# Performance work log

Measured on AMD Instinct MI355X. Metric: run time of the kernel, lower is better.

## Reference

```python
import jax, jax.numpy as jnp
import numpy as np

N = 5000
NFEAT = 512
NHID = 64
NHEADS = 8
NCLASS = 40
ALPHA = 0.2  # leaky relu slope
NEG_INF = -9e15


def setup_inputs() -> dict:
    key = jax.random.key(0)
    ks = jax.random.split(key, 12)
    x = jax.random.normal(ks[0], (N, NFEAT), dtype=jnp.float32)
    # binary adjacency, ~32 avg degree, with self loops
    adj = (jax.random.uniform(ks[1], (N, N)) < (32.0 / N)).astype(jnp.float32)
    adj = jnp.maximum(adj, jnp.eye(N, dtype=jnp.float32))
    s = 1.0 / np.sqrt(NFEAT)
    W_h = jax.random.uniform(ks[2], (NHEADS, NFEAT, NHID), minval=-s, maxval=s, dtype=jnp.float32)
    a_h = jax.random.uniform(ks[3], (NHEADS, 2 * NHID), minval=-s, maxval=s, dtype=jnp.float32)
    s2 = 1.0 / np.sqrt(NHID * NHEADS)
    W_o = jax.random.uniform(ks[4], (NHID * NHEADS, NHID), minval=-s2, maxval=s2, dtype=jnp.float32)
    a_o = jax.random.uniform(ks[5], (2 * NHID,), minval=-s2, maxval=s2, dtype=jnp.float32)
    s3 = 1.0 / np.sqrt(NHID)
    fc1_w = jax.random.uniform(ks[6], (NHID, 200), minval=-s3, maxval=s3, dtype=jnp.float32)
    fc1_b = jax.random.uniform(ks[7], (200,), minval=-s3, maxval=s3, dtype=jnp.float32)
    s4 = 1.0 / np.sqrt(200)
    fc2_w = jax.random.uniform(ks[8], (200, NCLASS), minval=-s4, maxval=s4, dtype=jnp.float32)
    fc2_b = jax.random.uniform(ks[9], (NCLASS,), minval=-s4, maxval=s4, dtype=jnp.float32)
    return {"x": x, "adj": adj, "W_h": W_h, "a_h": a_h, "W_o": W_o, "a_o": a_o,
            "fc1_w": fc1_w, "fc1_b": fc1_b, "fc2_w": fc2_w, "fc2_b": fc2_b}


def _masked_attention(e, adj):
    # e: [..., N, N]; mask where adj == 0, then row softmax
    e = jnp.where(adj > 0, e, NEG_INF)
    return jax.nn.softmax(e, axis=-1)


def reference(x, adj, W_h, a_h, W_o, a_o, fc1_w, fc1_b, fc2_w, fc2_b):
    # ---- multi-head GAT layer (concat=True), eval mode (dropout off) ----
    Wh = jnp.einsum('nf,hfo->hno', x, W_h)                 # [H, N, nhid]
    f1 = jnp.einsum('hno,ho->hn', Wh, a_h[:, :NHID])       # [H, N]
    f2 = jnp.einsum('hno,ho->hn', Wh, a_h[:, NHID:])       # [H, N]
    e = jax.nn.leaky_relu(f1[:, :, None] + f2[:, None, :], ALPHA)  # [H, N, N]
    att = _masked_attention(e, adj[None, :, :])
    h = jnp.einsum('hnm,hmo->hno', att, Wh)                # [H, N, nhid]
    h1 = jax.nn.elu(h).transpose(1, 0, 2).reshape(N, NHEADS * NHID)  # concat heads

    # ---- output GAT layer (concat=False) ----
    Wh2 = h1 @ W_o                                         # [N, nhid]
    g1 = Wh2 @ a_o[:NHID]                                  # [N]
    g2 = Wh2 @ a_o[NHID:]                                  # [N]
    e2 = jax.nn.leaky_relu(g1[:, None] + g2[None, :], ALPHA)
    att2 = _masked_attention(e2, adj)
    h2 = att2 @ Wh2                                        # [N, nhid]

    # ---- MLP head ----
    h3 = jax.nn.elu(h2 @ fc1_w + fc1_b)
    return h3 @ fc2_w + fc2_b                              # [N, nclass]
```

## Files before the change

kernel.cpp:

```cpp
#include <hip/hip_runtime.h>

typedef unsigned short u16;
typedef unsigned int u32;
typedef unsigned long long u64;
typedef __bf16 bf16_t;
typedef __bf16 bf16x8 __attribute__((ext_vector_type(8)));
typedef float f32x4 __attribute__((ext_vector_type(4)));
typedef u32 u32x4 __attribute__((ext_vector_type(4)));

#define NN 5000
#define NF 512
#define NH 64
#define HEADS 8
#define NCLS 40
#define CAP 128
#define LRELU 0.2f
#define BMW 80

#define CVT_BIG 320
#define BM_BLKS 1250
#define CVT_GRID (CVT_BIG + 8 + BM_BLKS)

__device__ __forceinline__ bool adj_is_bf16(const void* adj) {
    return ((*(const u32*)adj) & 0xFFFFu) != 0u;
}
__device__ __forceinline__ u16 rne_bf16(float f) {
    u32 u = __float_as_uint(f);
    u += 0x7FFFu + ((u >> 16) & 1u);
    return (u16)(u >> 16);
}
__device__ __forceinline__ float up_bf16(u16 h) {
    return __uint_as_float((u32)h << 16);
}
__device__ __forceinline__ u32x4 ntload4(const void* p, int idx) {
    return __builtin_nontemporal_load(((const u32x4*)p) + idx);
}

__global__ __launch_bounds__(256) void cvt(const void* __restrict__ x, const void* __restrict__ W_h,
                                           const void* __restrict__ adj,
                                           const void* a_h, const void* W_o, const void* a_o,
                                           const void* f1w, const void* f1b,
                                           const void* f2w, const void* f2b,
                                           u16* __restrict__ xc, u16* __restrict__ whc,
                                           float* a_hc, float* W_oc, float* a_oc,
                                           float* f1wc, float* f1bc, float* f2wc, float* f2bc,
                                           u64* __restrict__ bm) {
    const bool isb = adj_is_bf16(adj);
    const int b = blockIdx.x;
    if (b < CVT_BIG) {
        const int X4 = NN * NF / 4;
        const int T4 = X4 + HEADS * NF * NH / 4;
        for (int i = b * 256 + threadIdx.x; i < T4; i += CVT_BIG * 256) {
            const void* src; u16* dst; int off;
            if (i < X4) { src = x; dst = xc; off = i; }
            else        { src = W_h; dst = whc; off = i - X4; }
            ushort4 o;
            if (isb) {
                o = ((const ushort4*)src)[off];
            } else {
                u32x4 vv = ntload4(src, off);
                o.x = rne_bf16(__uint_as_float(vv[0])); o.y = rne_bf16(__uint_as_float(vv[1]));
                o.z = rne_bf16(__uint_as_float(vv[2])); o.w = rne_bf16(__uint_as_float(vv[3]));
            }
            ((ushort4*)dst)[off] = o;
        }
    } else if (b < CVT_BIG + 8) {
        const int s0 = HEADS * 2 * NH, s1 = HEADS * NH * NH, s2 = 2 * NH,
                  s3 = NH * 200, s4 = 200, s5 = 200 * NCLS, s6 = NCLS;
        const int total = s0 + s1 + s2 + s3 + s4 + s5 + s6;
        for (int i = (b - CVT_BIG) * 256 + threadIdx.x; i < total; i += 8 * 256) {
            const void* src; float* dst; int off = i;
            if (off < s0) { src = a_h; dst = a_hc; }
            else if ((off -= s0) < s1) { src = W_o;  dst = W_oc; }
            else if ((off -= s1) < s2) { src = a_o;  dst = a_oc; }
            else if ((off -= s2) < s3) { src = f1w;  dst = f1wc; }
            else if ((off -= s3) < s4) { src = f1b;  dst = f1bc; }
            else if ((off -= s4) < s5) { src = f2w;  dst = f2wc; }
            else { off -= s5;           src = f2b;  dst = f2bc; }
            dst[off] = isb ? up_bf16(((const u16*)src)[off]) : ((const float*)src)[off];
        }
    } else {
        const int lane = threadIdx.x & 63;
        const int wid  = threadIdx.x >> 6;
        const int r = (b - CVT_BIG - 8) * 4 + wid;
        u64* bmrow = bm + (size_t)r * BMW;
        if (!isb) {
            const float* row = (const float*)adj + (size_t)r * NN;
            #pragma unroll
            for (int pass = 0; pass < 2; ++pass) {
                u32x4 v[10];
                #pragma unroll
                for (int k = 0; k < 10; ++k) {
                    int c = (pass * 10 + k) * 64 + lane;
                    v[k] = (c < 1250) ? ntload4(row, c) : (u32x4){0u, 0u, 0u, 0u};
                }
                #pragma unroll
                for (int k = 0; k < 10; ++k) {
                    int i = pass * 10 + k;
                    #pragma unroll
                    for (int j = 0; j < 4; ++j) {
                        u64 m = __ballot(v[k][j] != 0u);
                        if (lane == j) bmrow[i * 4 + j] = m;
                    }
                }
            }
        } else {
            const u16* row = (const u16*)adj + (size_t)r * NN;
            u32x4 v[10];
            #pragma unroll
            for (int k = 0; k < 10; ++k) {
                int c = k * 64 + lane;
                v[k] = (c < 625) ? ntload4(row, c) : (u32x4){0u, 0u, 0u, 0u};
            }
            #pragma unroll
            for (int k = 0; k < 10; ++k) {
                #pragma unroll
                for (int j = 0; j < 4; ++j) {
                    u64 mlo = __ballot((v[k][j] & 0xFFFFu) != 0u);
                    u64 mhi = __ballot((v[k][j] >> 16) != 0u);
                    if (lane == 2 * j)     bmrow[k * 8 + 2 * j]     = mlo;
                    if (lane == 2 * j + 1) bmrow[k * 8 + 2 * j + 1] = mhi;
                }
            }
        }
    }
}

__global__ __launch_bounds__(256) void gemm1_f(const bf16_t* __restrict__ x,
                                               const bf16_t* __restrict__ W_h,
                                               const float* __restrict__ a_h,
                                               float* __restrict__ Wh,
                                               float* __restrict__ f1,
                                               float* __restrict__ f2) {
    const int lane = threadIdx.x & 63;
    const int wid  = threadIdx.x >> 6;
    const int rg = blockIdx.x;
    const int h  = blockIdx.y;
    const int quad = lane >> 4;
    const int lr   = lane & 15;
    const int kq   = quad * 8;
    const int nCol = wid * 16 + lr;
    const bf16_t* Bh = W_h + (size_t)h * NF * NH;
    __shared__ float f1s[4][64], f2s[4][64];

    bf16x8 bfrag[16];
    #pragma unroll
    for (int s = 0; s < 16; ++s) {
        bf16x8 bb;
        #pragma unroll
        for (int j = 0; j < 8; ++j) bb[j] = Bh[(s * 32 + kq + j) * NH + nCol];
        bfrag[s] = bb;
    }
    const float a1c = a_h[h * 128 + nCol];
    const float a2c = a_h[h * 128 + NH + nCol];

    for (int t = 0; t < 4; ++t) {
        const int rb = rg * 64 + t * 16;
        int row  = rb + lr;
        int rowc = row < NN ? row : NN - 1;
        const bf16_t* xp = x + (size_t)rowc * NF + kq;
        f32x4 acc = {0.f, 0.f, 0.f, 0.f};
        #pragma unroll
        for (int s = 0; s < 16; ++s) {
            bf16x8 a = *(const bf16x8*)(xp + s * 32);
            acc = __builtin_amdgcn_mfma_f32_16x16x32_bf16(a, bfrag[s], acc, 0, 0, 0);
        }
        #pragma unroll
        for (int r = 0; r < 4; ++r) {
            int gr = rb + quad * 4 + r;
            if (gr < NN) Wh[(size_t)gr * (HEADS * NH) + h * NH + nCol] = acc[r];
            float p1 = acc[r] * a1c, p2 = acc[r] * a2c;
            #pragma unroll
            for (int o = 8; o; o >>= 1) { p1 += __shfl_xor(p1, o); p2 += __shfl_xor(p2, o); }
            if (lr == 0) { f1s[wid][t * 16 + quad * 4 + r] = p1; f2s[wid][t * 16 + quad * 4 + r] = p2; }
        }
    }
    __syncthreads();
    if (wid == 0) {
        int gr = rg * 64 + lane;
        if (gr < NN) {
            f1[h * NN + gr] = f1s[0][lane] + f1s[1][lane] + f1s[2][lane] + f1s[3][lane];
            f2[h * NN + gr] = f2s[0][lane] + f2s[1][lane] + f2s[2][lane] + f2s[3][lane];
        }
    }
}

__global__ __launch_bounds__(256) void agg1f(const void* __restrict__ adj,
                                             const u64* __restrict__ bm,
                                             const float* __restrict__ Wh,
                                             const float* __restrict__ f1,
                                             const float* __restrict__ f2,
                                             int* __restrict__ nbr, int* __restrict__ deg,
                                             float* __restrict__ h1) {
    const bool isb = adj_is_bf16(adj);
    const int lane = threadIdx.x & 63;
    const int wid  = threadIdx.x >> 6;
    const int n = blockIdx.x;
    __shared__ int s_nbr[CAP];
    __shared__ int s_dall;

    if (wid == 0) {
        const u64* bmrow = bm + (size_t)n * BMW;
        int base = 0;
        #pragma unroll
        for (int r2 = 0; r2 < 2; ++r2) {
            int w = r2 * 64 + lane;
            u64 mw = (w < BMW) ? bmrow[w] : 0ull;
            int pc = __popcll(mw);
            int scan = pc;
            #pragma unroll
            for (int o = 1; o < 64; o <<= 1) {
                int t = __shfl_up(scan, o);
                if (lane >= o) scan += t;
            }
            int off = base + scan - pc;
            while (mw) {
                int bb = __ffsll(mw) - 1;
                mw &= mw - 1;
                int elem;
                if (!isb) elem = ((w >> 2) * 64 + bb) * 4 + (w & 3);
                else      elem = ((w >> 3) * 64 + bb) * 8 + (w & 7);
                if (off < CAP) s_nbr[off] = elem;
                ++off;
            }
            base += __shfl(scan, 63);
        }
        if (lane == 0) s_dall = base < CAP ? base : CAP;
    }
    __syncthreads();
    const int dall = s_dall;
    for (int i = threadIdx.x; i < dall; i += 256) nbr[(size_t)n * CAP + i] = s_nbr[i];
    if (threadIdx.x == 0) deg[n] = dall;

    const int ha = wid, hb = wid + 4;
    const int nb0 = (lane < dall) ? s_nbr[lane] : 0;
    const int nb1 = (lane + 64 < dall) ? s_nbr[lane + 64] : 0;
    const float f10 = f1[ha * NN + n], f11 = f1[hb * NN + n];
    const float* f2ha = f2 + (size_t)ha * NN;
    const float* f2hb = f2 + (size_t)hb * NN;

    float e00 = -INFINITY, e01 = -INFINITY, e10 = -INFINITY, e11 = -INFINITY;
    if (lane < dall) {
        float a = f10 + f2ha[nb0]; e00 = a > 0.f ? a : LRELU * a;
        float b = f11 + f2hb[nb0]; e10 = b > 0.f ? b : LRELU * b;
    }
    if (lane + 64 < dall) {
        float a = f10 + f2ha[nb1]; e01 = a > 0.f ? a : LRELU * a;
        float b = f11 + f2hb[nb1]; e11 = b > 0.f ? b : LRELU * b;
    }
    float mx0 = fmaxf(e00, e01), mx1 = fmaxf(e10, e11);
    #pragma unroll
    for (int o = 32; o; o >>= 1) {
        mx0 = fmaxf(mx0, __shfl_xor(mx0, o));
        mx1 = fmaxf(mx1, __shfl_xor(mx1, o));
    }
    float p00 = lane < dall ? expf(e00 - mx0) : 0.f;
    float p01 = lane + 64 < dall ? expf(e01 - mx0) : 0.f;
    float p10 = lane < dall ? expf(e10 - mx1) : 0.f;
    float p11 = lane + 64 < dall ? expf(e11 - mx1) : 0.f;
    float sm0 = p00 + p01, sm1 = p10 + p11;
    #pragma unroll
    for (int o = 32; o; o >>= 1) { sm0 += __shfl_xor(sm0, o); sm1 += __shfl_xor(sm1, o); }

    float A0 = 0.f, A1 = 0.f, A2 = 0.f, A3 = 0.f;
    float B0 = 0.f, B1 = 0.f, B2 = 0.f, B3 = 0.f;
    const float* W0 = Wh + ha * NH + lane;
    const float* W1 = Wh + hb * NH + lane;
    int j = 0;
    for (; j + 4 <= dall; j += 4) {
        #pragma unroll
        for (int i = 0; i < 4; ++i) {
            int jj = j + i;
            int sl = jj & 63;
            bool lo = jj < 64;
            int   m  = lo ? __shfl(nb0, sl) : __shfl(nb1, sl);
            float a0 = lo ? __shfl(p00, sl) : __shfl(p01, sl);
            float a1 = lo ? __shfl(p10, sl) : __shfl(p11, sl);
            size_t base = (size_t)m * (HEADS * NH);
            float w0 = W0[base], w1 = W1[base];
            if (i == 0) { A0 += a0 * w0; B0 += a1 * w1; }
            else if (i == 1) { A1 += a0 * w0; B1 += a1 * w1; }
            else if (i == 2) { A2 += a0 * w0; B2 += a1 * w1; }
            else { A3 += a0 * w0; B3 += a1 * w1; }
        }
    }
    for (; j < dall; ++j) {
        int sl = j & 63;
        bool lo = j < 64;
        int   m  = lo ? __shfl(nb0, sl) : __shfl(nb1, sl);
        float a0 = lo ? __shfl(p00, sl) : __shfl(p01, sl);
        float a1 = lo ? __shfl(p10, sl) : __shfl(p11, sl);
        size_t base = (size_t)m * (HEADS * NH);
        A0 += a0 * W0[base]; B0 += a1 * W1[base];
    }
    float hv0 = (A0 + A1 + A2 + A3) / sm0;
    float hv1 = (B0 + B1 + B2 + B3) / sm1;
    hv0 = hv0 > 0.f ? hv0 : expf(hv0) - 1.f;
    hv1 = hv1 > 0.f ? hv1 : expf(hv1) - 1.f;
    h1[(size_t)n * (HEADS * NH) + ha * NH + lane] = hv0;
    h1[(size_t)n * (HEADS * NH) + hb * NH + lane] = hv1;
}

__global__ __launch_bounds__(256) void gemm2_4(const float* __restrict__ h1,
                                               const float* __restrict__ W_o,
                                               const float* __restrict__ a_o,
                                               float* __restrict__ Wh2,
                                               float* __restrict__ g1,
                                               float* __restrict__ g2) {
    const int t = threadIdx.x;
    const int n0 = blockIdx.x * 4;
    __shared__ float sh[4 * 512];
    __shared__ float ps[4][4][64];
    const float4* src = (const float4*)(h1 + (size_t)n0 * 512);
    ((float4*)sh)[t]       = src[t];
    ((float4*)sh)[t + 256] = src[t + 256];
    __syncthreads();
    const int o = t & 63, part = t >> 6;
    float a0 = 0.f, a1 = 0.f, a2 = 0.f, a3 = 0.f;
    const float* wo = W_o + part * 128 * 64 + o;
    const float* s0 = sh + part * 128;
    #pragma unroll 4
    for (int f = 0; f < 128; ++f) {
        float w = wo[f * 64];
        a0 += s0[f] * w; a1 += s0[512 + f] * w; a2 += s0[1024 + f] * w; a3 += s0[1536 + f] * w;
    }
    ps[part][0][o] = a0; ps[part][1][o] = a1; ps[part][2][o] = a2; ps[part][3][o] = a3;
    __syncthreads();
    const int nd = t >> 6;
    float w2 = ps[0][nd][o] + ps[1][nd][o] + ps[2][nd][o] + ps[3][nd][o];
    Wh2[(size_t)(n0 + nd) * 64 + o] = w2;
    float p1 = w2 * a_o[o], p2 = w2 * a_o[64 + o];
    #pragma unroll
    for (int s = 32; s; s >>= 1) { p1 += __shfl_xor(p1, s); p2 += __shfl_xor(p2, s); }
    if (o == 0) { g1[n0 + nd] = p1; g2[n0 + nd] = p2; }
}

__global__ __launch_bounds__(256) void agg2_mlp(const float* __restrict__ Wh2,
                                                const float* __restrict__ g1,
                                                const float* __restrict__ g2,
                                                const int* __restrict__ nbr,
                                                const int* __restrict__ deg,
                                                const float* __restrict__ fc1_w,
                                                const float* __restrict__ fc1_b,
                                                const float* __restrict__ fc2_w,
                                                const float* __restrict__ fc2_b,
                                                float* __restrict__ out) {
    const int lane = threadIdx.x & 63;
    const int wid  = threadIdx.x >> 6;
    const int t = threadIdx.x;
    const int n0 = blockIdx.x * 4;
    const int n = n0 + wid;
    __shared__ float s_alpha[4][CAP];
    __shared__ int   s_nbr[4][CAP];
    __shared__ float s_h2[4][NH];
    __shared__ float s_h3[4][200];
    __shared__ float ps2[2][4][NCLS];
    const int d = deg[n];
    const int* nb = nbr + (size_t)n * CAP;
    const float gn = g1[n];

    float mx = -INFINITY;
    for (int j = lane; j < d; j += 64) {
        int m = nb[j];
        s_nbr[wid][j] = m;
        float e = gn + g2[m];
        e = e > 0.f ? e : LRELU * e;
        s_alpha[wid][j] = e;
        mx = fmaxf(mx, e);
    }
    #pragma unroll
    for (int o = 32; o; o >>= 1) mx = fmaxf(mx, __shfl_xor(mx, o));
    float sm = 0.f;
    for (int j = lane; j < d; j += 64) {
        float p = expf(s_alpha[wid][j] - mx);
        s_alpha[wid][j] = p;
        sm += p;
    }
    #pragma unroll
    for (int o = 32; o; o >>= 1) sm += __shfl_xor(sm, o);

    float acc0 = 0.f, acc1 = 0.f, acc2 = 0.f, acc3 = 0.f;
    int j = 0;
    for (; j + 4 <= d; j += 4) {
        acc0 += s_alpha[wid][j]     * Wh2[(size_t)s_nbr[wid][j]     * NH + lane];
        acc1 += s_alpha[wid][j + 1] * Wh2[(size_t)s_nbr[wid][j + 1] * NH + lane];
        acc2 += s_alpha[wid][j + 2] * Wh2[(size_t)s_nbr[wid][j + 2] * NH + lane];
        acc3 += s_alpha[wid][j + 3] * Wh2[(size_t)s_nbr[wid][j + 3] * NH + lane];
    }
    for (; j < d; ++j) acc0 += s_alpha[wid][j] * Wh2[(size_t)s_nbr[wid][j] * NH + lane];
    s_h2[wid][lane] = (acc0 + acc1 + acc2 + acc3) / sm;
    __syncthreads();

    if (t < 200) {
        float b0 = 0.f, b1 = 0.f, b2 = 0.f, b3 = 0.f;
        #pragma unroll 4
        for (int f = 0; f < NH; ++f) {
            float w = fc1_w[f * 200 + t];
            b0 += s_h2[0][f] * w; b1 += s_h2[1][f] * w; b2 += s_h2[2][f] * w; b3 += s_h2[3][f] * w;
        }
        float bb = fc1_b[t];
        b0 += bb; b1 += bb; b2 += bb; b3 += bb;
        s_h3[0][t] = b0 > 0.f ? b0 : expf(b0) - 1.f;
        s_h3[1][t] = b1 > 0.f ? b1 : expf(b1) - 1.f;
        s_h3[2][t] = b2 > 0.f ? b2 : expf(b2) - 1.f;
        s_h3[3][t] = b3 > 0.f ? b3 : expf(b3) - 1.f;
    }
    __syncthreads();

    if (t < 80) {
        const int o = t % 40, fh = t / 40;
        float c0 = 0.f, c1 = 0.f, c2 = 0.f, c3 = 0.f;
        #pragma unroll 4
        for (int f = fh * 100; f < fh * 100 + 100; ++f) {
            float w = fc2_w[f * NCLS + o];
            c0 += s_h3[0][f] * w; c1 += s_h3[1][f] * w; c2 += s_h3[2][f] * w; c3 += s_h3[3][f] * w;
        }
        ps2[fh][0][o] = c0; ps2[fh][1][o] = c1; ps2[fh][2][o] = c2; ps2[fh][3][o] = c3;
    }
    __syncthreads();
    if (t < 160) {
        const int nd = t / 40, o = t % 40;
        out[(size_t)(n0 + nd) * NCLS + o] = ps2[0][nd][o] + ps2[1][nd][o] + fc2_b[o];
    }
}

extern "C" void kernel_launch(void* const* d_in, const int* in_sizes, int n_in,
                              void* d_out, int out_size, void* d_ws, size_t ws_size,
                              hipStream_t stream) {
    const void* x     = d_in[0];
    const void* adj   = d_in[1];
    const void* W_h   = d_in[2];
    const void* a_h   = d_in[3];
    const void* W_o   = d_in[4];
    const void* a_o   = d_in[5];
    const void* fc1_w = d_in[6];
    const void* fc1_b = d_in[7];
    const void* fc2_w = d_in[8];
    const void* fc2_b = d_in[9];
    float* out = (float*)d_out;

    char* ws = (char*)d_ws;
    int*   nbr   = (int*)(ws + 0);
    int*   deg   = (int*)(ws + 2560000);
    float* Wh    = (float*)(ws + 2580000);
    float* f1    = (float*)(ws + 12820000);
    float* f2    = (float*)(ws + 12980000);
    float* h1    = (float*)(ws + 13140000);
    float* Wh2   = (float*)(ws + 23380000);
    float* g1    = (float*)(ws + 24660000);
    float* g2    = (float*)(ws + 24680000);
    u16*   xc    = (u16*)(ws + 24700000);
    u16*   whc   = (u16*)(ws + 29820000);
    float* a_hc  = (float*)(ws + 30344288);
    float* W_oc  = (float*)(ws + 30348384);
    float* a_oc  = (float*)(ws + 30479456);
    float* f1wc  = (float*)(ws + 30479968);
    float* f1bc  = (float*)(ws + 30531168);
    float* f2wc  = (float*)(ws + 30531968);
    float* f2bc  = (float*)(ws + 30563968);
    u64*   bm    = (u64*)(ws + 30564128);

    cvt<<<CVT_GRID, 256, 0, stream>>>(x, W_h, adj, a_h, W_o, a_o,
                                      fc1_w, fc1_b, fc2_w, fc2_b,
                                      xc, whc, a_hc, W_oc, a_oc,
                                      f1wc, f1bc, f2wc, f2bc, bm);
    gemm1_f<<<dim3(79, HEADS), 256, 0, stream>>>((const bf16_t*)xc, (const bf16_t*)whc,
                                                 a_hc, Wh, f1, f2);
    agg1f<<<NN, 256, 0, stream>>>(adj, bm, Wh, f1, f2, nbr, deg, h1);
    gemm2_4<<<NN / 4, 256, 0, stream>>>(h1, W_oc, a_oc, Wh2, g1, g2);
    agg2_mlp<<<NN / 4, 256, 0, stream>>>(Wh2, g1, g2, nbr, deg,
                                         f1wc, f1bc, f2wc, f2bc, out);
}
```

Before: 277.6 us.

## Fuse second-layer projection into first-layer aggregation kernel

Merges the per-node W_o projection and the g1/g2 attention logits into the first GAT aggregation kernel. Each block keeps its node's concatenated h1 row in shared memory instead of writing it to global memory, and the separate gemm2 launch is removed. This saves the 10MB h1 round trip and one launch. In exchange each block now multiplies a single node against W_o, reading the whole 128KB W_o per node where the old kernel reused it across four nodes. That puts more pressure on L2 and adds a sync.

Result: no change. 282.2 us (+1.7%).

```diff
diff --git a/kernel.cpp b/kernel.cpp
--- a/kernel.cpp
+++ b/kernel.cpp
@@ -185,19 +185,25 @@
     }
 }
 
-__global__ __launch_bounds__(256) void agg1f(const void* __restrict__ adj,
+__global__ __launch_bounds__(256) void agg1g(const void* __restrict__ adj,
                                              const u64* __restrict__ bm,
                                              const float* __restrict__ Wh,
                                              const float* __restrict__ f1,
                                              const float* __restrict__ f2,
+                                             const float* __restrict__ W_o,
+                                             const float* __restrict__ a_o,
                                              int* __restrict__ nbr, int* __restrict__ deg,
-                                             float* __restrict__ h1) {
+                                             float* __restrict__ Wh2,
+                                             float* __restrict__ g1, float* __restrict__ g2) {
     const bool isb = adj_is_bf16(adj);
     const int lane = threadIdx.x & 63;
     const int wid  = threadIdx.x >> 6;
+    const int t = threadIdx.x;
     const int n = blockIdx.x;
-    __shared__ int s_nbr[CAP];
-    __shared__ int s_dall;
+    __shared__ int   s_nbr[CAP];
+    __shared__ int   s_dall;
+    __shared__ float s_h1[HEADS * NH];
+    __shared__ float s_ps[4][NH];
 
     if (wid == 0) {
         const u64* bmrow = bm + (size_t)n * BMW;
@@ -210,8 +216,8 @@
             int scan = pc;
             #pragma unroll
             for (int o = 1; o < 64; o <<= 1) {
-                int t = __shfl_up(scan, o);
-                if (lane >= o) scan += t;
+                int tt = __shfl_up(scan, o);
+                if (lane >= o) scan += tt;
             }
             int off = base + scan - pc;
             while (mw) {
@@ -229,8 +235,8 @@
     }
     __syncthreads();
     const int dall = s_dall;
-    for (int i = threadIdx.x; i < dall; i += 256) nbr[(size_t)n * CAP + i] = s_nbr[i];
-    if (threadIdx.x == 0) deg[n] = dall;
+    for (int i = t; i < dall; i += 256) nbr[(size_t)n * CAP + i] = s_nbr[i];
+    if (t == 0) deg[n] = dall;
 
     const int ha = wid, hb = wid + 4;
     const int nb0 = (lane < dall) ? s_nbr[lane] : 0;
@@ -297,42 +303,26 @@
     float hv1 = (B0 + B1 + B2 + B3) / sm1;
     hv0 = hv0 > 0.f ? hv0 : expf(hv0) - 1.f;
     hv1 = hv1 > 0.f ? hv1 : expf(hv1) - 1.f;
-    h1[(size_t)n * (HEADS * NH) + ha * NH + lane] = hv0;
-    h1[(size_t)n * (HEADS * NH) + hb * NH + lane] = hv1;
-}
-
-__global__ __launch_bounds__(256) void gemm2_4(const float* __restrict__ h1,
-                                               const float* __restrict__ W_o,
-                                               const float* __restrict__ a_o,
-                                               float* __restrict__ Wh2,
-                                               float* __restrict__ g1,
-                                               float* __restrict__ g2) {
-    const int t = threadIdx.x;
-    const int n0 = blockIdx.x * 4;
-    __shared__ float sh[4 * 512];
-    __shared__ float ps[4][4][64];
-    const float4* src = (const float4*)(h1 + (size_t)n0 * 512);
-    ((float4*)sh)[t]       = src[t];
-    ((float4*)sh)[t + 256] = src[t + 256];
-    __syncthreads();
+    s_h1[ha * NH + lane] = hv0;
+    s_h1[hb * NH + lane] = hv1;
+    __syncthreads();
+
     const int o = t & 63, part = t >> 6;
-    float a0 = 0.f, a1 = 0.f, a2 = 0.f, a3 = 0.f;
+    float acc = 0.f;
     const float* wo = W_o + part * 128 * 64 + o;
-    const float* s0 = sh + part * 128;
+    const float* sp = s_h1 + part * 128;
     #pragma unroll 4
-    for (int f = 0; f < 128; ++f) {
-        float w = wo[f * 64];
-        a0 += s0[f] * w; a1 += s0[512 + f] * w; a2 += s0[1024 + f] * w; a3 += s0[1536 + f] * w;
-    }
-    ps[part][0][o] = a0; ps[part][1][o] = a1; ps[part][2][o] = a2; ps[part][3][o] = a3;
-    __syncthreads();
-    const int nd = t >> 6;
-    float w2 = ps[0][nd][o] + ps[1][nd][o] + ps[2][nd][o] + ps[3][nd][o];
-    Wh2[(size_t)(n0 + nd) * 64 + o] = w2;
-    float p1 = w2 * a_o[o], p2 = w2 * a_o[64 + o];
-    #pragma unroll
-    for (int s = 32; s; s >>= 1) { p1 += __shfl_xor(p1, s); p2 += __shfl_xor(p2, s); }
-    if (o == 0) { g1[n0 + nd] = p1; g2[n0 + nd] = p2; }
+    for (int f = 0; f < 128; ++f) acc += sp[f] * wo[f * 64];
+    s_ps[part][o] = acc;
+    __syncthreads();
+    if (t < 64) {
+        float w2 = s_ps[0][t] + s_ps[1][t] + s_ps[2][t] + s_ps[3][t];
+        Wh2[(size_t)n * NH + t] = w2;
+        float p1 = w2 * a_o[t], p2 = w2 * a_o[NH + t];
+        #pragma unroll
+        for (int s = 32; s; s >>= 1) { p1 += __shfl_xor(p1, s); p2 += __shfl_xor(p2, s); }
+        if (t == 0) { g1[n] = p1; g2[n] = p2; }
+    }
 }
 
 __global__ __launch_bounds__(256) void agg2_mlp(const float* __restrict__ Wh2,
@@ -445,20 +435,19 @@
     float* Wh    = (float*)(ws + 2580000);
     float* f1    = (float*)(ws + 12820000);
     float* f2    = (float*)(ws + 12980000);
-    float* h1    = (float*)(ws + 13140000);
-    float* Wh2   = (float*)(ws + 23380000);
-    float* g1    = (float*)(ws + 24660000);
-    float* g2    = (float*)(ws + 24680000);
-    u16*   xc    = (u16*)(ws + 24700000);
-    u16*   whc   = (u16*)(ws + 29820000);
-    float* a_hc  = (float*)(ws + 30344288);
-    float* W_oc  = (float*)(ws + 30348384);
-    float* a_oc  = (float*)(ws + 30479456);
-    float* f1wc  = (float*)(ws + 30479968);
-    float* f1bc  = (float*)(ws + 30531168);
-    float* f2wc  = (float*)(ws + 30531968);
-    float* f2bc  = (float*)(ws + 30563968);
-    u64*   bm    = (u64*)(ws + 30564128);
+    float* Wh2   = (float*)(ws + 13140000);
+    float* g1    = (float*)(ws + 14420000);
+    float* g2    = (float*)(ws + 14440000);
+    u16*   xc    = (u16*)(ws + 14460000);
+    u16*   whc   = (u16*)(ws + 19580000);
+    float* a_hc  = (float*)(ws + 20104288);
+    float* W_oc  = (float*)(ws + 20108384);
+    float* a_oc  = (float*)(ws + 20239456);
+    float* f1wc  = (float*)(ws + 20239968);
+    float* f1bc  = (float*)(ws + 20291168);
+    float* f2wc  = (float*)(ws + 20291968);
+    float* f2bc  = (float*)(ws + 20323968);
+    u64*   bm    = (u64*)(ws + 20324128);
 
     cvt<<<CVT_GRID, 256, 0, stream>>>(x, W_h, adj, a_h, W_o, a_o,
                                       fc1_w, fc1_b, fc2_w, fc2_b,
@@ -466,8 +455,8 @@
                                       f1wc, f1bc, f2wc, f2bc, bm);
     gemm1_f<<<dim3(79, HEADS), 256, 0, stream>>>((const bf16_t*)xc, (const bf16_t*)whc,
                                                  a_hc, Wh, f1, f2);
-    agg1f<<<NN, 256, 0, stream>>>(adj, bm, Wh, f1, f2, nbr, deg, h1);
-    gemm2_4<<<NN / 4, 256, 0, stream>>>(h1, W_oc, a_oc, Wh2, g1, g2);
+    agg1g<<<NN, 256, 0, stream>>>(adj, bm, Wh, f1, f2, W_oc, a_oc,
+                                  nbr, deg, Wh2, g1, g2);
     agg2_mlp<<<NN / 4, 256, 0, stream>>>(Wh2, g1, g2, nbr, deg,
                                          f1wc, f1bc, f2wc, f2bc, out);
 }
```
